# Optimization experiments

Measured on AMD Instinct MI355X. Metric: run time of the kernel, lower is better.

The kernel has to match this reference:

```python
import jax, jax.numpy as jnp
import numpy as np

NUM_HEADS = 4
LN_EPS = 1e-5


def setup_inputs() -> dict:
    key = jax.random.key(0)
    ks = jax.random.split(key, 5)
    C = 256
    x = jax.random.normal(ks[0], (2, C, 64, 64), dtype=jnp.float32)
    in_proj_w = jax.random.normal(ks[1], (3 * C, C), dtype=jnp.float32) * (1.0 / np.sqrt(C))
    in_proj_b = jax.random.normal(ks[2], (3 * C,), dtype=jnp.float32) * 0.02
    out_w = jax.random.normal(ks[3], (C, C), dtype=jnp.float32) * (1.0 / np.sqrt(C))
    out_b = jax.random.normal(ks[4], (C,), dtype=jnp.float32) * 0.02
    ln_g = jnp.ones((C,), dtype=jnp.float32)
    ln_b = jnp.zeros((C,), dtype=jnp.float32)
    return {"x": x, "in_proj_w": in_proj_w, "in_proj_b": in_proj_b,
            "out_w": out_w, "out_b": out_b, "ln_g": ln_g, "ln_b": ln_b}


def reference(x, in_proj_w, in_proj_b, out_w, out_b, ln_g, ln_b):
    b, c, H, W = x.shape
    S = H * W  # 4096 == max_tokens -> no pooling, no interpolation
    hd = c // NUM_HEADS
    t = x.reshape(b, c, S).transpose(0, 2, 1)  # (b, S, c)
    # fused QKV projection (in_proj_weight is [3c, c], rows = q,k,v blocks)
    qkv = t @ in_proj_w.T + in_proj_b  # (b, S, 3c)
    q, k, v = jnp.split(qkv, 3, axis=-1)
    def to_heads(a):
        return a.reshape(b, S, NUM_HEADS, hd).transpose(0, 2, 1, 3)  # (b, h, S, d)
    q = to_heads(q) * (1.0 / np.sqrt(hd))
    k = to_heads(k)
    v = to_heads(v)
    scores = jnp.einsum('bhqd,bhkd->bhqk', q, k)      # (b, h, S, S)
    probs = jax.nn.softmax(scores, axis=-1)
    attn = jnp.einsum('bhqk,bhkd->bhqd', probs, v)    # (b, h, S, d)
    attn = attn.transpose(0, 2, 1, 3).reshape(b, S, c)
    out = attn @ out_w.T + out_b                      # output projection
    # LayerNorm over channel dim
    mu = jnp.mean(out, axis=-1, keepdims=True)
    var = jnp.mean(jnp.square(out - mu), axis=-1, keepdims=True)
    out = (out - mu) * jax.lax.rsqrt(var + LN_EPS) * ln_g + ln_b
    return out.transpose(0, 2, 1).reshape(b, c, H, W)
```

## Files before the change

kernel.cpp:

```cpp
#include <hip/hip_runtime.h>
#include <cstddef>

#define S_TOK 4096
#define CDIM 256
#define NHEADS 4
#define HDIM 64
#define LSK 72
#define LDA 36
#define LDY 264
#define LOG2E 1.44269504f

typedef __attribute__((ext_vector_type(8))) short short8;
typedef __attribute__((ext_vector_type(4))) float floatx4;

__device__ inline unsigned short f2bf(float f) {
  union { float f; unsigned u; } v;
  v.f = f;
  unsigned r = v.u + 0x7fff + ((v.u >> 16) & 1);
  return (unsigned short)(r >> 16);
}
__device__ inline float bf2f(unsigned short u) {
  union { unsigned u; float f; } v;
  v.u = ((unsigned)u) << 16;
  return v.f;
}

__global__ __launch_bounds__(256) void convert_w_kernel(
    const float* __restrict__ ipw, const float* __restrict__ ow,
    unsigned short* __restrict__ wbf, unsigned short* __restrict__ owbf) {
  int idx = blockIdx.x * 256 + threadIdx.x;
  float4 f;
  unsigned short* dst;
  if (idx < 49152) {
    f = ((const float4*)ipw)[idx];
    dst = wbf + idx * 4;
  } else {
    int j = idx - 49152;
    f = ((const float4*)ow)[j];
    dst = owbf + j * 4;
  }
  ushort4 u;
  u.x = f2bf(f.x); u.y = f2bf(f.y); u.z = f2bf(f.z); u.w = f2bf(f.w);
  *(ushort4*)dst = u;
}

__global__ __launch_bounds__(256) void transpose_x_kernel(
    const float* __restrict__ x, unsigned short* __restrict__ xbfT) {
  __shared__ __align__(16) unsigned short T[64 * 72];
  const int tid = threadIdx.x;
  const int s0 = blockIdx.x * 64, c0 = blockIdx.y * 64, b = blockIdx.z;
  const int c_l = tid >> 2, q4 = tid & 3;
  const float4* src = (const float4*)(x + (((size_t)(b * CDIM + c0 + c_l)) << 12) + s0);
#pragma unroll
  for (int i = 0; i < 4; ++i) {
    int chunk = i * 4 + q4;
    float4 f = src[chunk];
    T[(chunk * 4 + 0) * 72 + c_l] = f2bf(f.x);
    T[(chunk * 4 + 1) * 72 + c_l] = f2bf(f.y);
    T[(chunk * 4 + 2) * 72 + c_l] = f2bf(f.z);
    T[(chunk * 4 + 3) * 72 + c_l] = f2bf(f.w);
  }
  __syncthreads();
  const int s_l = tid >> 2;
  unsigned short* drow = xbfT + ((size_t)((b << 12) + s0 + s_l)) * CDIM + c0;
#pragma unroll
  for (int i = 0; i < 2; ++i) {
    int chunk = i * 4 + q4;
    uint4 u = *(const uint4*)&T[s_l * 72 + chunk * 8];
    *(uint4*)(drow + chunk * 8) = u;
  }
}

__global__ __launch_bounds__(256) void qkv_gemm_kernel(
    const unsigned short* __restrict__ xbfT, const unsigned short* __restrict__ wbf,
    const float* __restrict__ ipb, unsigned short* __restrict__ q16,
    unsigned short* __restrict__ k16, unsigned short* __restrict__ vt16) {
  __shared__ __align__(16) unsigned short As[128 * LDA];
  __shared__ __align__(16) unsigned short Bs[64 * LDA];
  const int tid = threadIdx.x;
  const int wave = tid >> 6, lane = tid & 63;
  const int quad = lane >> 4, l16 = lane & 15;
  const int n0 = blockIdx.x * 64;
  const int tok0 = blockIdx.y * 128;
  const int b = blockIdx.z;

  const int r1 = tid >> 2, c1 = tid & 3;
  const unsigned short* gA = xbfT + ((size_t)(b * S_TOK + tok0 + r1)) * CDIM + c1 * 8;
  const unsigned short* gB = wbf + ((size_t)(n0 + r1)) * CDIM + c1 * 8;
  unsigned short* wA = &As[r1 * LDA + c1 * 8];
  unsigned short* wB = &Bs[r1 * LDA + c1 * 8];

  floatx4 acc[2][4];
#pragma unroll
  for (int mt = 0; mt < 2; ++mt)
#pragma unroll
    for (int nt = 0; nt < 4; ++nt) acc[mt][nt] = (floatx4){0.f, 0.f, 0.f, 0.f};

  uint4 a0p = *(const uint4*)(gA);
  uint4 a1p = *(const uint4*)(gA + 64 * CDIM);
  uint4 b0p = *(const uint4*)(gB);

  for (int ks = 0; ks < 8; ++ks) {
    __syncthreads();
    *(uint4*)wA = a0p;
    *(uint4*)(wA + 64 * LDA) = a1p;
    *(uint4*)wB = b0p;
    __syncthreads();
    if (ks < 7) {
      int off = (ks + 1) * 32;
      a0p = *(const uint4*)(gA + off);
      a1p = *(const uint4*)(gA + 64 * CDIM + off);
      b0p = *(const uint4*)(gB + off);
    }
    short8 af[2], bf[4];
#pragma unroll
    for (int mt = 0; mt < 2; ++mt)
      af[mt] = *(const short8*)&As[(wave * 32 + mt * 16 + l16) * LDA + quad * 8];
#pragma unroll
    for (int nt = 0; nt < 4; ++nt)
      bf[nt] = *(const short8*)&Bs[(nt * 16 + l16) * LDA + quad * 8];
#pragma unroll
    for (int mt = 0; mt < 2; ++mt)
#pragma unroll
      for (int nt = 0; nt < 4; ++nt)
        acc[mt][nt] = __builtin_amdgcn_mfma_f32_16x16x32_bf16(af[mt], bf[nt], acc[mt][nt], 0, 0, 0);
  }

  const int slab = n0 >> 8;
  int cb[4];
  float bias4[4];
#pragma unroll
  for (int nt = 0; nt < 4; ++nt) {
    cb[nt] = n0 + nt * 16 + l16;
    bias4[nt] = ipb[cb[nt]];
  }
  if (slab == 2) {
#pragma unroll
    for (int mt = 0; mt < 2; ++mt) {
      int tok = tok0 + wave * 32 + mt * 16 + quad * 4;
#pragma unroll
      for (int nt = 0; nt < 4; ++nt) {
        int dh = cb[nt] & 63, h = (cb[nt] >> 6) & 3;
        ushort4 u;
        u.x = f2bf(acc[mt][nt][0] + bias4[nt]);
        u.y = f2bf(acc[mt][nt][1] + bias4[nt]);
        u.z = f2bf(acc[mt][nt][2] + bias4[nt]);
        u.w = f2bf(acc[mt][nt][3] + bias4[nt]);
        *(ushort4*)&vt16[((size_t)((b * NHEADS + h) * HDIM + dh)) * S_TOK + tok] = u;
      }
    }
  } else {
    unsigned short* dst = slab ? k16 : q16;
    const float sc = slab ? 1.0f : 0.125f * LOG2E;
#pragma unroll
    for (int mt = 0; mt < 2; ++mt)
#pragma unroll
      for (int nt = 0; nt < 4; ++nt) {
        int dh = cb[nt] & 63, h = (cb[nt] >> 6) & 3;
        size_t base = ((size_t)(b * NHEADS + h) * S_TOK);
#pragma unroll
        for (int r = 0; r < 4; ++r) {
          int tok = tok0 + wave * 32 + mt * 16 + quad * 4 + r;
          dst[(base + tok) * HDIM + dh] = f2bf((acc[mt][nt][r] + bias4[nt]) * sc);
        }
      }
  }
}

__global__ __launch_bounds__(256) void attn_kernel(
    const unsigned short* __restrict__ q16,
    const unsigned short* __restrict__ k16,
    const unsigned short* __restrict__ vt16,
    unsigned short* __restrict__ op, float* __restrict__ lp) {
  __shared__ __align__(16) unsigned short Ks[64 * LSK];
  __shared__ __align__(16) unsigned short Vt[64 * LSK];
  __shared__ __align__(16) unsigned short Ps[4 * 32 * LSK];

  const int tid = threadIdx.x;
  const int wave = tid >> 6;
  const int lane = tid & 63;
  const int quad = lane >> 4;
  const int l16 = lane & 15;
  const int bh = blockIdx.y;
  const int q0 = blockIdx.x * 128;
  const int split = blockIdx.z;
  const int kt0 = split * 16;

  short8 qf[2][2];
#pragma unroll
  for (int mt = 0; mt < 2; ++mt) {
    const unsigned short* qg =
        q16 + ((size_t)bh * S_TOK + q0 + wave * 32 + mt * 16 + l16) * HDIM + quad * 8;
    qf[mt][0] = *(const short8*)(qg);
    qf[mt][1] = *(const short8*)(qg + 32);
  }

  const int sr = tid >> 3, scc = tid & 7;
  const unsigned short* kg = k16 + ((size_t)bh * S_TOK + sr) * HDIM + scc * 8;
  const unsigned short* vg = vt16 + ((size_t)bh * HDIM + sr) * S_TOK + scc * 8;
  unsigned short* ksw = &Ks[sr * LSK + scc * 8];
  unsigned short* vtw = &Vt[sr * LSK + scc * 8];

  floatx4 O[2][4];
  float lsum[2][4];
#pragma unroll
  for (int mt = 0; mt < 2; ++mt)
#pragma unroll
    for (int nt = 0; nt < 4; ++nt) O[mt][nt] = (floatx4){0.f, 0.f, 0.f, 0.f};
#pragma unroll
  for (int mt = 0; mt < 2; ++mt)
#pragma unroll
    for (int r = 0; r < 4; ++r) lsum[mt][r] = 0.f;

  uint4 k0r = *(const uint4*)(kg + (size_t)kt0 * 64 * HDIM);
  uint4 k1r = *(const uint4*)(kg + (size_t)kt0 * 64 * HDIM + 32 * HDIM);
  uint4 v0r = *(const uint4*)(vg + kt0 * 64);
  uint4 v1r = *(const uint4*)(vg + kt0 * 64 + (size_t)32 * S_TOK);

  for (int t = 0; t < 16; ++t) {
    __syncthreads();
    *(uint4*)ksw = k0r;
    *(uint4*)(ksw + 32 * LSK) = k1r;
    *(uint4*)vtw = v0r;
    *(uint4*)(vtw + 32 * LSK) = v1r;
    __syncthreads();
    if (t < 15) {
      const unsigned short* kgn = kg + (size_t)(kt0 + t + 1) * 64 * HDIM;
      const unsigned short* vgn = vg + (kt0 + t + 1) * 64;
      k0r = *(const uint4*)(kgn);
      k1r = *(const uint4*)(kgn + 32 * HDIM);
      v0r = *(const uint4*)(vgn);
      v1r = *(const uint4*)(vgn + (size_t)32 * S_TOK);
    }

    floatx4 sc[2][4];
#pragma unroll
    for (int nt = 0; nt < 4; ++nt) {
      short8 kf0 = *(const short8*)(&Ks[(nt * 16 + l16) * LSK + quad * 8]);
      short8 kf1 = *(const short8*)(&Ks[(nt * 16 + l16) * LSK + 32 + quad * 8]);
#pragma unroll
      for (int mt = 0; mt < 2; ++mt) {
        floatx4 c = (floatx4){0.f, 0.f, 0.f, 0.f};
        c = __builtin_amdgcn_mfma_f32_16x16x32_bf16(qf[mt][0], kf0, c, 0, 0, 0);
        c = __builtin_amdgcn_mfma_f32_16x16x32_bf16(qf[mt][1], kf1, c, 0, 0, 0);
        sc[mt][nt] = c;
      }
    }

    unsigned short* pw = &Ps[(wave * 32) * LSK];
#pragma unroll
    for (int mt = 0; mt < 2; ++mt)
#pragma unroll
      for (int nt = 0; nt < 4; ++nt)
#pragma unroll
        for (int r = 0; r < 4; ++r) {
          float p = __builtin_amdgcn_exp2f(sc[mt][nt][r]);
          lsum[mt][r] += p;
          pw[(mt * 16 + quad * 4 + r) * LSK + nt * 16 + l16] = f2bf(p);
        }

    short8 pf[2][2];
#pragma unroll
    for (int mt = 0; mt < 2; ++mt) {
      pf[mt][0] = *(const short8*)(&pw[(mt * 16 + l16) * LSK + quad * 8]);
      pf[mt][1] = *(const short8*)(&pw[(mt * 16 + l16) * LSK + 32 + quad * 8]);
    }
#pragma unroll
    for (int nt = 0; nt < 4; ++nt) {
      short8 vf0 = *(const short8*)(&Vt[(nt * 16 + l16) * LSK + quad * 8]);
      short8 vf1 = *(const short8*)(&Vt[(nt * 16 + l16) * LSK + 32 + quad * 8]);
#pragma unroll
      for (int mt = 0; mt < 2; ++mt) {
        O[mt][nt] = __builtin_amdgcn_mfma_f32_16x16x32_bf16(pf[mt][0], vf0, O[mt][nt], 0, 0, 0);
        O[mt][nt] = __builtin_amdgcn_mfma_f32_16x16x32_bf16(pf[mt][1], vf1, O[mt][nt], 0, 0, 0);
      }
    }
  }

  unsigned short* op_s = op + (size_t)split * 2097152;
  float* lp_s = lp + (size_t)split * 32768;
#pragma unroll
  for (int mt = 0; mt < 2; ++mt)
#pragma unroll
    for (int r = 0; r < 4; ++r) {
      float ls = lsum[mt][r];
      ls += __shfl_xor(ls, 1);
      ls += __shfl_xor(ls, 2);
      ls += __shfl_xor(ls, 4);
      ls += __shfl_xor(ls, 8);
      int row = q0 + wave * 32 + mt * 16 + quad * 4 + r;
#pragma unroll
      for (int nt = 0; nt < 4; ++nt)
        op_s[((size_t)bh * S_TOK + row) * HDIM + nt * 16 + l16] = f2bf(O[mt][nt][r]);
      if (l16 == 0) lp_s[bh * S_TOK + row] = ls;
    }
}

__global__ __launch_bounds__(256) void merge_kernel(
    const unsigned short* __restrict__ op, const float* __restrict__ lp,
    unsigned short* __restrict__ ab16) {
  int idx = blockIdx.x * 256 + threadIdx.x;
  int row = idx >> 3;
  int ch = idx & 7;
  float rinv = 1.0f / (lp[row] + lp[32768 + row] + lp[65536 + row] + lp[98304 + row]);
  float s[8];
#pragma unroll
  for (int i = 0; i < 8; ++i) s[i] = 0.f;
#pragma unroll
  for (int sp = 0; sp < 4; ++sp) {
    uint4 a = *(const uint4*)(op + (size_t)sp * 2097152 + (size_t)row * HDIM + ch * 8);
    const unsigned* au = (const unsigned*)&a;
#pragma unroll
    for (int i = 0; i < 4; ++i) {
      s[i * 2] += bf2f((unsigned short)(au[i] & 0xffff));
      s[i * 2 + 1] += bf2f((unsigned short)(au[i] >> 16));
    }
  }
  ushort4 o[2];
#pragma unroll
  for (int i = 0; i < 8; ++i) ((unsigned short*)o)[i] = f2bf(s[i] * rinv);
  int bh = row >> 12, tok = row & 4095;
  int b = bh >> 2, h = bh & 3;
  unsigned short* dst = ab16 + ((size_t)(b * S_TOK + tok)) * CDIM + h * HDIM + ch * 8;
  *(ushort4*)dst = o[0];
  *(ushort4*)(dst + 4) = o[1];
}

__global__ __launch_bounds__(256) void out_ln_gemm_kernel(
    const unsigned short* __restrict__ ab16, const unsigned short* __restrict__ owbf,
    const float* __restrict__ obias, const float* __restrict__ lng,
    const float* __restrict__ lnb, float* __restrict__ out) {
  __shared__ __align__(16) unsigned short As[16 * LDA];
  __shared__ __align__(16) unsigned short Bs[256 * LDA];
  __shared__ __align__(16) float ys[16 * LDY];
  const int tid = threadIdx.x;
  const int wave = tid >> 6, lane = tid & 63;
  const int quad = lane >> 4, l16 = lane & 15;
  const int tok0 = blockIdx.x * 16;

  const int ar = tid >> 4, ac = tid & 15;
  const unsigned short* gA = ab16 + ((size_t)(tok0 + ar)) * CDIM + ac * 2;
  unsigned short* wAp = &As[ar * LDA + ac * 2];
  const int br = tid >> 2, bc = tid & 3;
  const unsigned short* gB = owbf + ((size_t)br) * CDIM + bc * 8;
  unsigned short* wBp = &Bs[br * LDA + bc * 8];

  floatx4 acc[4];
#pragma unroll
  for (int nt = 0; nt < 4; ++nt) acc[nt] = (floatx4){0.f, 0.f, 0.f, 0.f};

  unsigned ap = *(const unsigned*)(gA);
  uint4 bp[4];
#pragma unroll
  for (int i = 0; i < 4; ++i) bp[i] = *(const uint4*)(gB + (size_t)i * 64 * CDIM);

  for (int ks = 0; ks < 8; ++ks) {
    __syncthreads();
    *(unsigned*)wAp = ap;
#pragma unroll
    for (int i = 0; i < 4; ++i) *(uint4*)(wBp + i * 64 * LDA) = bp[i];
    __syncthreads();
    if (ks < 7) {
      int off = (ks + 1) * 32;
      ap = *(const unsigned*)(gA + off);
#pragma unroll
      for (int i = 0; i < 4; ++i)
        bp[i] = *(const uint4*)(gB + (size_t)i * 64 * CDIM + off);
    }
    short8 af = *(const short8*)&As[l16 * LDA + quad * 8];
    short8 bf[4];
#pragma unroll
    for (int nt = 0; nt < 4; ++nt)
      bf[nt] = *(const short8*)&Bs[(wave * 64 + nt * 16 + l16) * LDA + quad * 8];
#pragma unroll
    for (int nt = 0; nt < 4; ++nt)
      acc[nt] = __builtin_amdgcn_mfma_f32_16x16x32_bf16(af, bf[nt], acc[nt], 0, 0, 0);
  }

#pragma unroll
  for (int nt = 0; nt < 4; ++nt) {
    int c = wave * 64 + nt * 16 + l16;
    float bo = obias[c];
#pragma unroll
    for (int r = 0; r < 4; ++r)
      ys[(quad * 4 + r) * LDY + c] = acc[nt][r] + bo;
  }
  __syncthreads();

  const int gtok = tid >> 4, lx = tid & 15;
  float sum = 0.f, ssq = 0.f;
#pragma unroll
  for (int i = 0; i < 16; ++i) {
    float v = ys[gtok * LDY + i * 16 + lx];
    sum += v;
    ssq += v * v;
  }
  sum += __shfl_xor(sum, 1); ssq += __shfl_xor(ssq, 1);
  sum += __shfl_xor(sum, 2); ssq += __shfl_xor(ssq, 2);
  sum += __shfl_xor(sum, 4); ssq += __shfl_xor(ssq, 4);
  sum += __shfl_xor(sum, 8); ssq += __shfl_xor(ssq, 8);
  float mu = sum * (1.f / 256.f);
  float var = ssq * (1.f / 256.f) - mu * mu;
  float rstd = rsqrtf(var + 1e-5f);
  const int b2 = tok0 >> 12;
  const int sl = (tok0 & 4095) + gtok;
#pragma unroll
  for (int i = 0; i < 16; ++i) {
    int c = i * 16 + lx;
    float v = ys[gtok * LDY + c];
    out[(((size_t)(b2 * CDIM + c)) << 12) + sl] = (v - mu) * rstd * lng[c] + lnb[c];
  }
}

extern "C" void kernel_launch(void* const* d_in, const int* in_sizes, int n_in,
                              void* d_out, int out_size, void* d_ws, size_t ws_size,
                              hipStream_t stream) {
  const float* x = (const float*)d_in[0];
  const float* ipw = (const float*)d_in[1];
  const float* ipb = (const float*)d_in[2];
  const float* ow = (const float*)d_in[3];
  const float* ob = (const float*)d_in[4];
  const float* lng = (const float*)d_in[5];
  const float* lnb = (const float*)d_in[6];
  float* out = (float*)d_out;
  unsigned short* wbf = (unsigned short*)d_ws;
  unsigned short* owbf = wbf + 196608;
  unsigned short* xbfT = owbf + 65536;
  unsigned short* q16 = xbfT + 2097152;
  unsigned short* k16 = q16 + 2097152;
  unsigned short* vt16 = k16 + 2097152;
  unsigned short* op = vt16 + 2097152;
  unsigned short* ab16 = op + 8388608;
  float* lp = (float*)(ab16 + 2097152);

  convert_w_kernel<<<256, 256, 0, stream>>>(ipw, ow, wbf, owbf);
  transpose_x_kernel<<<dim3(64, 4, 2), 256, 0, stream>>>(x, xbfT);
  qkv_gemm_kernel<<<dim3(12, 32, 2), 256, 0, stream>>>(xbfT, wbf, ipb, q16, k16, vt16);
  attn_kernel<<<dim3(32, 8, 4), 256, 0, stream>>>(q16, k16, vt16, op, lp);
  merge_kernel<<<1024, 256, 0, stream>>>(op, lp, ab16);
  out_ln_gemm_kernel<<<512, 256, 0, stream>>>(ab16, owbf, ob, lng, lnb, out);
}
```

Measured before the change: 173.5 us.

## Fuse prep kernels, transpose score MFMA, fold split merge into output GEMM

Merges the weight-conversion and x-transpose kernels into one launch. In attention, it swaps the MFMA operands so each lane holds four consecutive keys of a single query row. That lets the probabilities go to LDS as packed 8-byte stores and the row sums finish with two shuffles instead of four. The split-K merge kernel is removed: attention writes partial outputs in token-major head layout, and the output GEMM sums the four splits and normalises while loading its A tile. This saves two launches and an intermediate round trip, but the GEMM A-load now reads four times as much data.

Result: faster. 167.6 us (-3.4%).

```diff
diff --git a/kernel.cpp b/kernel.cpp
--- a/kernel.cpp
+++ b/kernel.cpp
@@ -25,30 +25,31 @@
   return v.f;
 }
 
-__global__ __launch_bounds__(256) void convert_w_kernel(
-    const float* __restrict__ ipw, const float* __restrict__ ow,
-    unsigned short* __restrict__ wbf, unsigned short* __restrict__ owbf) {
-  int idx = blockIdx.x * 256 + threadIdx.x;
-  float4 f;
-  unsigned short* dst;
-  if (idx < 49152) {
-    f = ((const float4*)ipw)[idx];
-    dst = wbf + idx * 4;
-  } else {
-    int j = idx - 49152;
-    f = ((const float4*)ow)[j];
-    dst = owbf + j * 4;
-  }
-  ushort4 u;
-  u.x = f2bf(f.x); u.y = f2bf(f.y); u.z = f2bf(f.z); u.w = f2bf(f.w);
-  *(ushort4*)dst = u;
-}
-
-__global__ __launch_bounds__(256) void transpose_x_kernel(
-    const float* __restrict__ x, unsigned short* __restrict__ xbfT) {
+__global__ __launch_bounds__(256) void prep_kernel(
+    const float* __restrict__ x, const float* __restrict__ ipw,
+    const float* __restrict__ ow, unsigned short* __restrict__ wbf,
+    unsigned short* __restrict__ owbf, unsigned short* __restrict__ xbfT) {
   __shared__ __align__(16) unsigned short T[64 * 72];
   const int tid = threadIdx.x;
-  const int s0 = blockIdx.x * 64, c0 = blockIdx.y * 64, b = blockIdx.z;
+  if (blockIdx.x < 256) {
+    int idx = blockIdx.x * 256 + tid;
+    float4 f;
+    unsigned short* dst;
+    if (idx < 49152) {
+      f = ((const float4*)ipw)[idx];
+      dst = wbf + idx * 4;
+    } else {
+      int j = idx - 49152;
+      f = ((const float4*)ow)[j];
+      dst = owbf + j * 4;
+    }
+    ushort4 u;
+    u.x = f2bf(f.x); u.y = f2bf(f.y); u.z = f2bf(f.z); u.w = f2bf(f.w);
+    *(ushort4*)dst = u;
+    return;
+  }
+  const int bid = blockIdx.x - 256;
+  const int s0 = (bid & 63) * 64, c0 = ((bid >> 6) & 3) * 64, b = bid >> 8;
   const int c_l = tid >> 2, q4 = tid & 3;
   const float4* src = (const float4*)(x + (((size_t)(b * CDIM + c0 + c_l)) << 12) + s0);
 #pragma unroll
@@ -202,20 +203,18 @@
   unsigned short* vtw = &Vt[sr * LSK + scc * 8];
 
   floatx4 O[2][4];
-  float lsum[2][4];
+  float lsum[2] = {0.f, 0.f};
 #pragma unroll
   for (int mt = 0; mt < 2; ++mt)
 #pragma unroll
     for (int nt = 0; nt < 4; ++nt) O[mt][nt] = (floatx4){0.f, 0.f, 0.f, 0.f};
-#pragma unroll
-  for (int mt = 0; mt < 2; ++mt)
-#pragma unroll
-    for (int r = 0; r < 4; ++r) lsum[mt][r] = 0.f;
 
   uint4 k0r = *(const uint4*)(kg + (size_t)kt0 * 64 * HDIM);
   uint4 k1r = *(const uint4*)(kg + (size_t)kt0 * 64 * HDIM + 32 * HDIM);
   uint4 v0r = *(const uint4*)(vg + kt0 * 64);
   uint4 v1r = *(const uint4*)(vg + kt0 * 64 + (size_t)32 * S_TOK);
+
+  unsigned short* pw = &Ps[(wave * 32) * LSK];
 
   for (int t = 0; t < 16; ++t) {
     __syncthreads();
@@ -233,31 +232,26 @@
       v1r = *(const uint4*)(vgn + (size_t)32 * S_TOK);
     }
 
-    floatx4 sc[2][4];
-#pragma unroll
-    for (int nt = 0; nt < 4; ++nt) {
-      short8 kf0 = *(const short8*)(&Ks[(nt * 16 + l16) * LSK + quad * 8]);
-      short8 kf1 = *(const short8*)(&Ks[(nt * 16 + l16) * LSK + 32 + quad * 8]);
+#pragma unroll
+    for (int kt = 0; kt < 4; ++kt) {
+      short8 kf0 = *(const short8*)(&Ks[(kt * 16 + l16) * LSK + quad * 8]);
+      short8 kf1 = *(const short8*)(&Ks[(kt * 16 + l16) * LSK + 32 + quad * 8]);
 #pragma unroll
       for (int mt = 0; mt < 2; ++mt) {
         floatx4 c = (floatx4){0.f, 0.f, 0.f, 0.f};
-        c = __builtin_amdgcn_mfma_f32_16x16x32_bf16(qf[mt][0], kf0, c, 0, 0, 0);
-        c = __builtin_amdgcn_mfma_f32_16x16x32_bf16(qf[mt][1], kf1, c, 0, 0, 0);
-        sc[mt][nt] = c;
+        c = __builtin_amdgcn_mfma_f32_16x16x32_bf16(kf0, qf[mt][0], c, 0, 0, 0);
+        c = __builtin_amdgcn_mfma_f32_16x16x32_bf16(kf1, qf[mt][1], c, 0, 0, 0);
+        float p0 = __builtin_amdgcn_exp2f(c[0]);
+        float p1 = __builtin_amdgcn_exp2f(c[1]);
+        float p2 = __builtin_amdgcn_exp2f(c[2]);
+        float p3 = __builtin_amdgcn_exp2f(c[3]);
+        lsum[mt] += (p0 + p1) + (p2 + p3);
+        uint2 pk;
+        pk.x = ((unsigned)f2bf(p1) << 16) | f2bf(p0);
+        pk.y = ((unsigned)f2bf(p3) << 16) | f2bf(p2);
+        *(uint2*)&pw[(mt * 16 + l16) * LSK + kt * 16 + quad * 4] = pk;
       }
     }
-
-    unsigned short* pw = &Ps[(wave * 32) * LSK];
-#pragma unroll
-    for (int mt = 0; mt < 2; ++mt)
-#pragma unroll
-      for (int nt = 0; nt < 4; ++nt)
-#pragma unroll
-        for (int r = 0; r < 4; ++r) {
-          float p = __builtin_amdgcn_exp2f(sc[mt][nt][r]);
-          lsum[mt][r] += p;
-          pw[(mt * 16 + quad * 4 + r) * LSK + nt * 16 + l16] = f2bf(p);
-        }
 
     short8 pf[2][2];
 #pragma unroll
@@ -277,69 +271,63 @@
     }
   }
 
+  const int b = bh >> 2, h = bh & 3;
   unsigned short* op_s = op + (size_t)split * 2097152;
   float* lp_s = lp + (size_t)split * 32768;
 #pragma unroll
-  for (int mt = 0; mt < 2; ++mt)
+  for (int mt = 0; mt < 2; ++mt) {
+    float ls = lsum[mt];
+    ls += __shfl_xor(ls, 16);
+    ls += __shfl_xor(ls, 32);
+    if (quad == 0)
+      lp_s[bh * S_TOK + q0 + wave * 32 + mt * 16 + l16] = ls;
 #pragma unroll
     for (int r = 0; r < 4; ++r) {
-      float ls = lsum[mt][r];
-      ls += __shfl_xor(ls, 1);
-      ls += __shfl_xor(ls, 2);
-      ls += __shfl_xor(ls, 4);
-      ls += __shfl_xor(ls, 8);
       int row = q0 + wave * 32 + mt * 16 + quad * 4 + r;
 #pragma unroll
       for (int nt = 0; nt < 4; ++nt)
-        op_s[((size_t)bh * S_TOK + row) * HDIM + nt * 16 + l16] = f2bf(O[mt][nt][r]);
-      if (l16 == 0) lp_s[bh * S_TOK + row] = ls;
-    }
-}
-
-__global__ __launch_bounds__(256) void merge_kernel(
+        op_s[((size_t)(b * S_TOK + row)) * CDIM + h * HDIM + nt * 16 + l16] =
+            f2bf(O[mt][nt][r]);
+    }
+  }
+}
+
+__device__ inline unsigned merge2(const unsigned short* op, size_t off, float rinv) {
+  float lo = 0.f, hi = 0.f;
+#pragma unroll
+  for (int sp = 0; sp < 4; ++sp) {
+    unsigned u = *(const unsigned*)(op + (size_t)sp * 2097152 + off);
+    lo += bf2f((unsigned short)(u & 0xffff));
+    hi += bf2f((unsigned short)(u >> 16));
+  }
+  return ((unsigned)f2bf(hi * rinv) << 16) | f2bf(lo * rinv);
+}
+
+__global__ __launch_bounds__(256) void out_ln_gemm_kernel(
     const unsigned short* __restrict__ op, const float* __restrict__ lp,
-    unsigned short* __restrict__ ab16) {
-  int idx = blockIdx.x * 256 + threadIdx.x;
-  int row = idx >> 3;
-  int ch = idx & 7;
-  float rinv = 1.0f / (lp[row] + lp[32768 + row] + lp[65536 + row] + lp[98304 + row]);
-  float s[8];
-#pragma unroll
-  for (int i = 0; i < 8; ++i) s[i] = 0.f;
-#pragma unroll
-  for (int sp = 0; sp < 4; ++sp) {
-    uint4 a = *(const uint4*)(op + (size_t)sp * 2097152 + (size_t)row * HDIM + ch * 8);
-    const unsigned* au = (const unsigned*)&a;
-#pragma unroll
-    for (int i = 0; i < 4; ++i) {
-      s[i * 2] += bf2f((unsigned short)(au[i] & 0xffff));
-      s[i * 2 + 1] += bf2f((unsigned short)(au[i] >> 16));
-    }
-  }
-  ushort4 o[2];
-#pragma unroll
-  for (int i = 0; i < 8; ++i) ((unsigned short*)o)[i] = f2bf(s[i] * rinv);
-  int bh = row >> 12, tok = row & 4095;
-  int b = bh >> 2, h = bh & 3;
-  unsigned short* dst = ab16 + ((size_t)(b * S_TOK + tok)) * CDIM + h * HDIM + ch * 8;
-  *(ushort4*)dst = o[0];
-  *(ushort4*)(dst + 4) = o[1];
-}
-
-__global__ __launch_bounds__(256) void out_ln_gemm_kernel(
-    const unsigned short* __restrict__ ab16, const unsigned short* __restrict__ owbf,
-    const float* __restrict__ obias, const float* __restrict__ lng,
-    const float* __restrict__ lnb, float* __restrict__ out) {
+    const unsigned short* __restrict__ owbf, const float* __restrict__ obias,
+    const float* __restrict__ lng, const float* __restrict__ lnb,
+    float* __restrict__ out) {
   __shared__ __align__(16) unsigned short As[16 * LDA];
   __shared__ __align__(16) unsigned short Bs[256 * LDA];
   __shared__ __align__(16) float ys[16 * LDY];
+  __shared__ float rsum[64];
   const int tid = threadIdx.x;
   const int wave = tid >> 6, lane = tid & 63;
   const int quad = lane >> 4, l16 = lane & 15;
   const int tok0 = blockIdx.x * 16;
 
+  if (tid < 64) {
+    int t = tid >> 2, h = tid & 3;
+    int bb = tok0 >> 12;
+    int idx = (bb * 4 + h) * 4096 + (tok0 & 4095) + t;
+    rsum[t * 4 + h] =
+        1.0f / (lp[idx] + lp[32768 + idx] + lp[65536 + idx] + lp[98304 + idx]);
+  }
+  __syncthreads();
+
   const int ar = tid >> 4, ac = tid & 15;
-  const unsigned short* gA = ab16 + ((size_t)(tok0 + ar)) * CDIM + ac * 2;
+  const size_t abase = (size_t)(tok0 + ar) * CDIM + ac * 2;
   unsigned short* wAp = &As[ar * LDA + ac * 2];
   const int br = tid >> 2, bc = tid & 3;
   const unsigned short* gB = owbf + ((size_t)br) * CDIM + bc * 8;
@@ -349,7 +337,7 @@
 #pragma unroll
   for (int nt = 0; nt < 4; ++nt) acc[nt] = (floatx4){0.f, 0.f, 0.f, 0.f};
 
-  unsigned ap = *(const unsigned*)(gA);
+  unsigned ap = merge2(op, abase, rsum[ar * 4]);
   uint4 bp[4];
 #pragma unroll
   for (int i = 0; i < 4; ++i) bp[i] = *(const uint4*)(gB + (size_t)i * 64 * CDIM);
@@ -362,7 +350,7 @@
     __syncthreads();
     if (ks < 7) {
       int off = (ks + 1) * 32;
-      ap = *(const unsigned*)(gA + off);
+      ap = merge2(op, abase + off, rsum[ar * 4 + ((ks + 1) >> 1)]);
 #pragma unroll
       for (int i = 0; i < 4; ++i)
         bp[i] = *(const uint4*)(gB + (size_t)i * 64 * CDIM + off);
@@ -430,13 +418,10 @@
   unsigned short* k16 = q16 + 2097152;
   unsigned short* vt16 = k16 + 2097152;
   unsigned short* op = vt16 + 2097152;
-  unsigned short* ab16 = op + 8388608;
-  float* lp = (float*)(ab16 + 2097152);
-
-  convert_w_kernel<<<256, 256, 0, stream>>>(ipw, ow, wbf, owbf);
-  transpose_x_kernel<<<dim3(64, 4, 2), 256, 0, stream>>>(x, xbfT);
+  float* lp = (float*)(op + 8388608);
+
+  prep_kernel<<<768, 256, 0, stream>>>(x, ipw, ow, wbf, owbf, xbfT);
   qkv_gemm_kernel<<<dim3(12, 32, 2), 256, 0, stream>>>(xbfT, wbf, ipb, q16, k16, vt16);
   attn_kernel<<<dim3(32, 8, 4), 256, 0, stream>>>(q16, k16, vt16, op, lp);
-  merge_kernel<<<1024, 256, 0, stream>>>(op, lp, ab16);
-  out_ln_gemm_kernel<<<512, 256, 0, stream>>>(ab16, owbf, ob, lng, lnb, out);
-}
+  out_ln_gemm_kernel<<<512, 256, 0, stream>>>(op, lp, owbf, ob, lng, lnb, out);
+}
```
